# Kernel optimization log

Measured on AMD Instinct MI355X. Metric: run time of the kernel, lower is better.

The kernel has to match this reference:

```python
import jax, jax.numpy as jnp
import numpy as np

B, S, D = 2, 2048, 1024
QKV = 2048
H = 16
HD = QKV // H  # 128
SCALE = HD ** -0.5


def setup_inputs() -> dict:
    key = jax.random.key(0)
    k1, k2, k3, k4, k5 = jax.random.split(key, 5)
    std = D ** -0.5
    return {
        "x": jax.random.normal(k1, (B, S, D), dtype=jnp.float32),
        "wq": jax.random.normal(k2, (QKV, D), dtype=jnp.float32) * std,
        "wk": jax.random.normal(k3, (QKV, D), dtype=jnp.float32) * std,
        "wv": jax.random.normal(k4, (QKV, D), dtype=jnp.float32) * std,
        "wo": jax.random.normal(k5, (D, QKV), dtype=jnp.float32) * (QKV ** -0.5),
    }


def reference(x, wq, wk, wv, wo):
    b, s, _ = x.shape
    # QKV projections (torch Linear: y = x @ W.T), reshape to [b, h, s, hd]
    q = (x @ wq.T).reshape(b, s, H, HD).transpose(0, 2, 1, 3)
    k = (x @ wk.T).reshape(b, s, H, HD).transpose(0, 2, 1, 3)
    v = (x @ wv.T).reshape(b, s, H, HD).transpose(0, 2, 1, 3)
    scores = jnp.einsum("bhqd,bhkd->bhqk", q, k) * SCALE
    causal = jnp.tril(jnp.ones((s, s), dtype=bool))
    scores = jnp.where(causal[None, None], scores, -jnp.inf)
    attn = jax.nn.softmax(scores, axis=-1)  # dropout p=0 (eval)
    out = jnp.einsum("bhqk,bhkd->bhqd", attn, v)
    out = out.transpose(0, 2, 1, 3).reshape(b, s, QKV)
    return out @ wo.T
```

## Files before the change

### kernel.cpp

```cpp
#include <hip/hip_runtime.h>
#include <hip/hip_bf16.h>
#include <cstdint>

#define SEQ   2048
#define DMOD  1024
#define QKVD  2048
#define NH    16
#define HDIM  128
#define NTOK  4096

typedef __bf16 bf16;
typedef bf16 bf16x4 __attribute__((ext_vector_type(4)));
typedef bf16 bf16x8 __attribute__((ext_vector_type(8)));
typedef float f32x4 __attribute__((ext_vector_type(4)));
typedef float f32x16 __attribute__((ext_vector_type(16)));
typedef uint32_t u32x4 __attribute__((ext_vector_type(4)));

typedef __attribute__((address_space(1))) void* as1_t;
typedef __attribute__((address_space(3))) void* as3_t;

__device__ __forceinline__ void gload16(const void* g, void* l) {
  __builtin_amdgcn_global_load_lds((as1_t)(uintptr_t)g, (as3_t)(uintptr_t)l, 16, 0, 0);
}

__device__ __forceinline__ uint32_t pkbf(float a, float b) {
  union { bf16 h; unsigned short u; } x, y;
  x.h = (bf16)a; y.h = (bf16)b;
  return (uint32_t)x.u | ((uint32_t)y.u << 16);
}

__device__ __forceinline__ void plswap(uint32_t& a, uint32_t& b) {
  asm("v_permlane32_swap_b32 %0, %1" : "+v"(a), "+v"(b));
}

__global__ void cast_f32_bf16(const float* __restrict__ in, bf16* __restrict__ out, int n4) {
  int i = blockIdx.x * blockDim.x + threadIdx.x;
  if (i < n4) {
    float4 v = reinterpret_cast<const float4*>(in)[i];
    bf16x4 o;
    o[0] = (bf16)v.x; o[1] = (bf16)v.y; o[2] = (bf16)v.z; o[3] = (bf16)v.w;
    reinterpret_cast<bf16x4*>(out)[i] = o;
  }
}

__global__ void cast_w4(const float* __restrict__ p0, const float* __restrict__ p1,
                        const float* __restrict__ p2, const float* __restrict__ p3,
                        bf16* __restrict__ out) {
  int i = blockIdx.x * blockDim.x + threadIdx.x;
  const float* src = (i < 524288) ? p0 : (i < 1048576) ? p1 : (i < 1572864) ? p2 : p3;
  int off = i & 524287;
  float4 v = reinterpret_cast<const float4*>(src)[off];
  bf16x4 o;
  o[0] = (bf16)v.x; o[1] = (bf16)v.y; o[2] = (bf16)v.z; o[3] = (bf16)v.w;
  reinterpret_cast<bf16x4*>(out)[i] = o;
}

__global__ __launch_bounds__(512, 1) void qkv_gemm_kernel(
    const bf16* __restrict__ A, const bf16* __restrict__ Bw,
    bf16* __restrict__ Qo, bf16* __restrict__ Ko, bf16* __restrict__ Vto, float qs)
{
  __shared__ bf16 RING[3][24576];

  const int tid  = threadIdx.x;
  const int lane = tid & 63;
  const int wid  = tid >> 6;
  const int wm   = wid >> 2;
  const int wn   = wid & 3;
  const int lm   = lane & 15;
  const int lg   = lane >> 4;

  const int g   = blockIdx.x & 7;
  const int idx = blockIdx.x >> 3;
  const int m0  = ((g & 1) * 16 + (idx & 15)) * 128;
  const int n0  = ((g >> 1) * 6 + (idx >> 4)) * 256;

  f32x4 acc[4][4];
#pragma unroll
  for (int i = 0; i < 4; ++i)
#pragma unroll
    for (int j = 0; j < 4; ++j) acc[i][j] = (f32x4)0.0f;

  const int rl = lane >> 3;
  const int cbb = (lane & 7) * 16;

  auto stageA = [&](int kt, int slot) {
    const int k0 = kt * 64;
    char* Ab = (char*)&RING[slot][0];
#pragma unroll
    for (int r2 = 0; r2 < 2; ++r2) {
      int chunk = r2 * 8 + wid;
      int row   = chunk * 8 + rl;
      int cx    = cbb ^ ((row & 7) << 4);
      gload16(A + (size_t)(m0 + row) * DMOD + k0 + (cx >> 1), Ab + chunk * 1024);
    }
  };
  auto stageB1 = [&](int kt, int slot, int r2) {
    const int k0 = kt * 64;
    char* Bb = (char*)&RING[slot][0] + 16384;
    int chunk = r2 * 8 + wid;
    int row   = chunk * 8 + rl;
    int cx    = cbb ^ ((row & 7) << 4);
    gload16(Bw + (size_t)(n0 + row) * DMOD + k0 + (cx >> 1), Bb + chunk * 1024);
  };
  auto stageFull = [&](int kt, int slot) {
    stageA(kt, slot);
#pragma unroll
    for (int r2 = 0; r2 < 4; ++r2) stageB1(kt, slot, r2);
  };

  auto rdA = [&](const char* Ab, int mf, int kk) -> bf16x8 {
    int row = wm * 64 + mf * 16 + lm;
    int cx  = (kk * 64 + lg * 16) ^ ((row & 7) << 4);
    return *(const bf16x8*)(Ab + row * 128 + cx);
  };
  auto rdB = [&](const char* Bb, int nf, int kk) -> bf16x8 {
    int row = wn * 64 + nf * 16 + lm;
    int cx  = (kk * 64 + lg * 16) ^ ((row & 7) << 4);
    return *(const bf16x8*)(Bb + row * 128 + cx);
  };

  stageFull(0, 0);
  stageFull(1, 1);

  int cur = 0;
  for (int t = 0; t < 16; ++t) {
    if (t < 15) asm volatile("s_waitcnt vmcnt(6)" ::: "memory");
    else        asm volatile("s_waitcnt vmcnt(0)" ::: "memory");
    __builtin_amdgcn_s_barrier();

    const char* Ab = (const char*)&RING[cur][0];
    const char* Bb = Ab + 16384;
    const bool pf = (t + 2 < 16);
    const int  ps = (cur + 2 >= 3) ? (cur - 1) : (cur + 2);

    bf16x8 a[4], b[2];

#pragma unroll
    for (int mf = 0; mf < 4; ++mf) a[mf] = rdA(Ab, mf, 0);
    b[0] = rdB(Bb, 0, 0); b[1] = rdB(Bb, 1, 0);
    if (pf) stageA(t + 2, ps);
    __builtin_amdgcn_s_barrier();
    asm volatile("s_waitcnt lgkmcnt(0)" ::: "memory");
    __builtin_amdgcn_s_setprio(1);
#pragma unroll
    for (int mf = 0; mf < 4; ++mf) {
      acc[mf][0] = __builtin_amdgcn_mfma_f32_16x16x32_bf16(a[mf], b[0], acc[mf][0], 0, 0, 0);
      acc[mf][1] = __builtin_amdgcn_mfma_f32_16x16x32_bf16(a[mf], b[1], acc[mf][1], 0, 0, 0);
    }
    __builtin_amdgcn_s_setprio(0);
    __builtin_amdgcn_s_barrier();

    b[0] = rdB(Bb, 2, 0); b[1] = rdB(Bb, 3, 0);
    if (pf) { stageB1(t + 2, ps, 0); stageB1(t + 2, ps, 1); }
    __builtin_amdgcn_s_barrier();
    asm volatile("s_waitcnt lgkmcnt(0)" ::: "memory");
    __builtin_amdgcn_s_setprio(1);
#pragma unroll
    for (int mf = 0; mf < 4; ++mf) {
      acc[mf][2] = __builtin_amdgcn_mfma_f32_16x16x32_bf16(a[mf], b[0], acc[mf][2], 0, 0, 0);
      acc[mf][3] = __builtin_amdgcn_mfma_f32_16x16x32_bf16(a[mf], b[1], acc[mf][3], 0, 0, 0);
    }
    __builtin_amdgcn_s_setprio(0);
    __builtin_amdgcn_s_barrier();

#pragma unroll
    for (int mf = 0; mf < 4; ++mf) a[mf] = rdA(Ab, mf, 1);
    b[0] = rdB(Bb, 0, 1); b[1] = rdB(Bb, 1, 1);
    if (pf) stageB1(t + 2, ps, 2);
    __builtin_amdgcn_s_barrier();
    asm volatile("s_waitcnt lgkmcnt(0)" ::: "memory");
    __builtin_amdgcn_s_setprio(1);
#pragma unroll
    for (int mf = 0; mf < 4; ++mf) {
      acc[mf][0] = __builtin_amdgcn_mfma_f32_16x16x32_bf16(a[mf], b[0], acc[mf][0], 0, 0, 0);
      acc[mf][1] = __builtin_amdgcn_mfma_f32_16x16x32_bf16(a[mf], b[1], acc[mf][1], 0, 0, 0);
    }
    __builtin_amdgcn_s_setprio(0);
    __builtin_amdgcn_s_barrier();

    b[0] = rdB(Bb, 2, 1); b[1] = rdB(Bb, 3, 1);
    if (pf) stageB1(t + 2, ps, 3);
    __builtin_amdgcn_s_barrier();
    asm volatile("s_waitcnt lgkmcnt(0)" ::: "memory");
    __builtin_amdgcn_s_setprio(1);
#pragma unroll
    for (int mf = 0; mf < 4; ++mf) {
      acc[mf][2] = __builtin_amdgcn_mfma_f32_16x16x32_bf16(a[mf], b[0], acc[mf][2], 0, 0, 0);
      acc[mf][3] = __builtin_amdgcn_mfma_f32_16x16x32_bf16(a[mf], b[1], acc[mf][3], 0, 0, 0);
    }
    __builtin_amdgcn_s_setprio(0);
    __builtin_amdgcn_s_barrier();

    cur = (cur == 2) ? 0 : cur + 1;
  }

#pragma unroll
  for (int mf = 0; mf < 4; ++mf) {
#pragma unroll
    for (int nf = 0; nf < 4; ++nf) {
      int row0 = m0 + wm * 64 + mf * 16 + lg * 4;
      int col  = n0 + wn * 64 + nf * 16 + lm;
      f32x4 cv = acc[mf][nf];
      if (n0 < 2048) {
#pragma unroll
        for (int r = 0; r < 4; ++r)
          Qo[(size_t)(row0 + r) * QKVD + col] = (bf16)(cv[r] * qs);
      } else if (n0 < 4096) {
        int kc = col - 2048;
#pragma unroll
        for (int r = 0; r < 4; ++r)
          Ko[(size_t)(row0 + r) * QKVD + kc] = (bf16)cv[r];
      } else {
        int vc = col - 4096;
#pragma unroll
        for (int r = 0; r < 4; ++r) {
          int tok = row0 + r; int bb = tok >> 11; int s = tok & 2047;
          Vto[((size_t)bb * QKVD + vc) * SEQ + s] = (bf16)cv[r];
        }
      }
    }
  }
}

__global__ __launch_bounds__(256, 2) void proj_kernel(
    const bf16* __restrict__ A, const bf16* __restrict__ Bw, float* __restrict__ out)
{
  __shared__ bf16 RING[2][16384];

  const int tid  = threadIdx.x;
  const int lane = tid & 63;
  const int wid  = tid >> 6;
  const int wm   = wid >> 1;
  const int wn   = wid & 1;
  const int lm   = lane & 15;
  const int lg   = lane >> 4;

  const int g   = blockIdx.x & 7;
  const int idx = blockIdx.x >> 3;
  const int m0  = (g * 4 + (idx >> 3)) * 128;
  const int n0  = (idx & 7) * 128;

  f32x4 acc[4][4];
#pragma unroll
  for (int i = 0; i < 4; ++i)
#pragma unroll
    for (int j = 0; j < 4; ++j) acc[i][j] = (f32x4)0.0f;

  const int rl = lane >> 3;
  const int cbb = (lane & 7) * 16;

  auto stage = [&](int kt, int slot) {
    const int k0 = kt * 64;
    char* Ab = (char*)&RING[slot][0];
    char* Bb = Ab + 16384;
#pragma unroll
    for (int r2 = 0; r2 < 4; ++r2) {
      int chunk = r2 * 4 + wid;
      int row   = chunk * 8 + rl;
      int cx    = cbb ^ ((row & 7) << 4);
      gload16(A + (size_t)(m0 + row) * QKVD + k0 + (cx >> 1), Ab + chunk * 1024);
    }
#pragma unroll
    for (int r2 = 0; r2 < 4; ++r2) {
      int chunk = r2 * 4 + wid;
      int row   = chunk * 8 + rl;
      int cx    = cbb ^ ((row & 7) << 4);
      gload16(Bw + (size_t)(n0 + row) * QKVD + k0 + (cx >> 1), Bb + chunk * 1024);
    }
  };

  auto rdA = [&](const char* Ab, int mf, int kk) -> bf16x8 {
    int row = wm * 64 + mf * 16 + lm;
    int cx  = (kk * 64 + lg * 16) ^ ((row & 7) << 4);
    return *(const bf16x8*)(Ab + row * 128 + cx);
  };
  auto rdB = [&](const char* Bb, int nf, int kk) -> bf16x8 {
    int row = wn * 64 + nf * 16 + lm;
    int cx  = (kk * 64 + lg * 16) ^ ((row & 7) << 4);
    return *(const bf16x8*)(Bb + row * 128 + cx);
  };

  stage(0, 0);

  int cur = 0;
  for (int t = 0; t < 32; ++t) {
    if (t < 31) {
      stage(t + 1, cur ^ 1);
      asm volatile("s_waitcnt vmcnt(8)" ::: "memory");
    } else {
      asm volatile("s_waitcnt vmcnt(0)" ::: "memory");
    }
    __builtin_amdgcn_s_barrier();

    const char* Ab = (const char*)&RING[cur][0];
    const char* Bb = Ab + 16384;

    bf16x8 a[4], b[2];

#pragma unroll
    for (int mf = 0; mf < 4; ++mf) a[mf] = rdA(Ab, mf, 0);
    b[0] = rdB(Bb, 0, 0); b[1] = rdB(Bb, 1, 0);
    __builtin_amdgcn_s_barrier();
    asm volatile("s_waitcnt lgkmcnt(0)" ::: "memory");
    __builtin_amdgcn_s_setprio(1);
#pragma unroll
    for (int mf = 0; mf < 4; ++mf) {
      acc[mf][0] = __builtin_amdgcn_mfma_f32_16x16x32_bf16(a[mf], b[0], acc[mf][0], 0, 0, 0);
      acc[mf][1] = __builtin_amdgcn_mfma_f32_16x16x32_bf16(a[mf], b[1], acc[mf][1], 0, 0, 0);
    }
    __builtin_amdgcn_s_setprio(0);
    __builtin_amdgcn_s_barrier();

    b[0] = rdB(Bb, 2, 0); b[1] = rdB(Bb, 3, 0);
    __builtin_amdgcn_s_barrier();
    asm volatile("s_waitcnt lgkmcnt(0)" ::: "memory");
    __builtin_amdgcn_s_setprio(1);
#pragma unroll
    for (int mf = 0; mf < 4; ++mf) {
      acc[mf][2] = __builtin_amdgcn_mfma_f32_16x16x32_bf16(a[mf], b[0], acc[mf][2], 0, 0, 0);
      acc[mf][3] = __builtin_amdgcn_mfma_f32_16x16x32_bf16(a[mf], b[1], acc[mf][3], 0, 0, 0);
    }
    __builtin_amdgcn_s_setprio(0);
    __builtin_amdgcn_s_barrier();

#pragma unroll
    for (int mf = 0; mf < 4; ++mf) a[mf] = rdA(Ab, mf, 1);
    b[0] = rdB(Bb, 0, 1); b[1] = rdB(Bb, 1, 1);
    __builtin_amdgcn_s_barrier();
    asm volatile("s_waitcnt lgkmcnt(0)" ::: "memory");
    __builtin_amdgcn_s_setprio(1);
#pragma unroll
    for (int mf = 0; mf < 4; ++mf) {
      acc[mf][0] = __builtin_amdgcn_mfma_f32_16x16x32_bf16(a[mf], b[0], acc[mf][0], 0, 0, 0);
      acc[mf][1] = __builtin_amdgcn_mfma_f32_16x16x32_bf16(a[mf], b[1], acc[mf][1], 0, 0, 0);
    }
    __builtin_amdgcn_s_setprio(0);
    __builtin_amdgcn_s_barrier();

    b[0] = rdB(Bb, 2, 1); b[1] = rdB(Bb, 3, 1);
    __builtin_amdgcn_s_barrier();
    asm volatile("s_waitcnt lgkmcnt(0)" ::: "memory");
    __builtin_amdgcn_s_setprio(1);
#pragma unroll
    for (int mf = 0; mf < 4; ++mf) {
      acc[mf][2] = __builtin_amdgcn_mfma_f32_16x16x32_bf16(a[mf], b[0], acc[mf][2], 0, 0, 0);
      acc[mf][3] = __builtin_amdgcn_mfma_f32_16x16x32_bf16(a[mf], b[1], acc[mf][3], 0, 0, 0);
    }
    __builtin_amdgcn_s_setprio(0);
    __builtin_amdgcn_s_barrier();

    cur ^= 1;
  }

#pragma unroll
  for (int mf = 0; mf < 4; ++mf)
#pragma unroll
    for (int nf = 0; nf < 4; ++nf) {
      int row0 = m0 + wm * 64 + mf * 16 + lg * 4;
      int col  = n0 + wn * 64 + nf * 16 + lm;
      f32x4 cv = acc[mf][nf];
#pragma unroll
      for (int r = 0; r < 4; ++r)
        out[(size_t)(row0 + r) * DMOD + col] = cv[r];
    }
}

__global__ __launch_bounds__(256, 2) void flash_kernel(
    const bf16* __restrict__ Q, const bf16* __restrict__ Kg,
    const bf16* __restrict__ Vt, bf16* __restrict__ O)
{
  __shared__ bf16 KV[2][16384];

  const int tid  = threadIdx.x;
  const int lane = tid & 63;
  const int wid  = tid >> 6;
  const int l31  = lane & 31;
  const int lh   = lane >> 5;

  const int id  = blockIdx.x;
  const int c   = id & 255;
  const int s   = id >> 8;
  const int bh  = (c & 7) * 4 + ((c >> 3) & 3);
  const int k   = (c >> 5) & 7;
  const int T   = s ? (15 - k) : k;
  const int nu  = 2 * (T + 1);
  const int b   = bh >> 4;
  const int h   = bh & 15;
  const int rA  = T * 128 + wid * 32;

  auto stage = [&](int j, int buf) {
    bf16* kb = &KV[buf][0];
    bf16* vb = &KV[buf][8192];
    const int rb0 = wid * 16;
#pragma unroll
    for (int i = 0; i < 4; ++i) {
      int r0 = rb0 + i * 4;
      int r  = r0 + (lane >> 4);
      int cc = ((lane & 15) * 16) ^ ((r & 15) << 4);
      gload16(Kg + ((size_t)(b * SEQ + j * 64 + r)) * QKVD + h * HDIM + (cc >> 1),
              kb + r0 * 128);
    }
    const int db0 = wid * 32;
#pragma unroll
    for (int i = 0; i < 4; ++i) {
      int d0 = db0 + i * 8;
      int d  = d0 + (lane >> 3);
      int cc = ((lane & 7) * 16) ^ ((d & 7) << 4);
      gload16(Vt + ((size_t)(bh * HDIM + d)) * SEQ + j * 64 + (cc >> 1),
              vb + d0 * 64);
    }
  };

  bf16x8 qfr[8];
  {
    const bf16* qb = Q + ((size_t)(b * SEQ + rA + l31)) * QKVD + h * HDIM + lh * 8;
#pragma unroll
    for (int st = 0; st < 8; ++st) qfr[st] = *reinterpret_cast<const bf16x8*>(qb + st * 16);
  }

  f32x16 o[4];
#pragma unroll
  for (int cc = 0; cc < 4; ++cc) o[cc] = (f32x16)0.0f;
  float mreg = -__builtin_inff();
  float lreg = 0.0f;

  stage(0, 0);
  __syncthreads();

  int cur = 0;
  for (int j = 0; j < nu; ++j) {
    if (j + 1 < nu) stage(j + 1, cur ^ 1);

    const bool act = (j * 64 <= rA + 31);
    if (act) {
      const char* kbb = (const char*)&KV[cur][0];
      const char* vbb = kbb + 16384;

      f32x16 s0 = (f32x16)0.0f, s1 = (f32x16)0.0f;
#pragma unroll
      for (int st = 0; st < 8; ++st) {
        const int r0 = l31, r1 = 32 + l31;
        bf16x8 kf0 = *(const bf16x8*)(kbb + r0 * 256 + ((lh * 16 + st * 32) ^ ((r0 & 15) << 4)));
        bf16x8 kf1 = *(const bf16x8*)(kbb + r1 * 256 + ((lh * 16 + st * 32) ^ ((r1 & 15) << 4)));
        s0 = __builtin_amdgcn_mfma_f32_32x32x16_bf16(kf0, qfr[st], s0, 0, 0, 0);
        s1 = __builtin_amdgcn_mfma_f32_32x32x16_bf16(kf1, qfr[st], s1, 0, 0, 0);
      }

      const bool full = (j * 64 + 63) <= rA;
      if (!full) {
        const int qr  = rA + l31;
        const int kb0 = j * 64 + 4 * lh;
#pragma unroll
        for (int r = 0; r < 16; ++r) {
          int key = kb0 + (r & 3) + 8 * (r >> 2);
          if (key > qr)      s0[r] = -1e30f;
          if (key + 32 > qr) s1[r] = -1e30f;
        }
      }

      float mx = s0[0];
#pragma unroll
      for (int r = 1; r < 16; ++r) mx = fmaxf(mx, s0[r]);
#pragma unroll
      for (int r = 0; r < 16; ++r) mx = fmaxf(mx, s1[r]);
      mx = fmaxf(mx, __shfl_xor(mx, 32));

      float mn;
      if (__all(mx <= mreg + 8.0f)) {
        mn = mreg;
      } else {
        mn = fmaxf(mreg, mx);
        float scl = exp2f(mreg - mn);
        mreg = mn;
        lreg *= scl;
#pragma unroll
        for (int r = 0; r < 16; ++r) {
          int row = (r & 3) + 8 * (r >> 2) + 4 * lh;
          float sr = __shfl(scl, row);
#pragma unroll
          for (int cc = 0; cc < 4; ++cc) o[cc][r] *= sr;
        }
      }

      float p[32];
#pragma unroll
      for (int r = 0; r < 16; ++r) p[r]      = exp2f(s0[r] - mn);
#pragma unroll
      for (int r = 0; r < 16; ++r) p[16 + r] = exp2f(s1[r] - mn);
      float rs = 0.0f;
#pragma unroll
      for (int r = 0; r < 32; ++r) rs += p[r];
      rs += __shfl_xor(rs, 32);
      lreg += rs;

      bf16x8 pa[4];
#pragma unroll
      for (int f = 0; f < 4; ++f) {
        const float* pp = p + f * 8;
        uint32_t w0 = pkbf(pp[0], pp[1]);
        uint32_t w1 = pkbf(pp[2], pp[3]);
        uint32_t w2 = pkbf(pp[4], pp[5]);
        uint32_t w3 = pkbf(pp[6], pp[7]);
        plswap(w0, w2);
        plswap(w1, w3);
        u32x4 w = {w0, w1, w2, w3};
        pa[f] = __builtin_bit_cast(bf16x8, w);
      }

#pragma unroll
      for (int cc = 0; cc < 4; ++cc) {
        const int d = cc * 32 + l31;
        const char* vrow = vbb + d * 128;
        const int dx = (d & 7) << 4;
#pragma unroll
        for (int f = 0; f < 4; ++f) {
          bf16x8 vf = *(const bf16x8*)(vrow + ((f * 32 + lh * 16) ^ dx));
          o[cc] = __builtin_amdgcn_mfma_f32_32x32x16_bf16(pa[f], vf, o[cc], 0, 0, 0);
        }
      }
    }

    __syncthreads();
    cur ^= 1;
  }

  float linv = 1.0f / lreg;
#pragma unroll
  for (int cc = 0; cc < 4; ++cc)
#pragma unroll
    for (int r = 0; r < 16; ++r) {
      int row = (r & 3) + 8 * (r >> 2) + 4 * lh;
      float li = __shfl(linv, row);
      O[((size_t)(b * SEQ + rA + row)) * QKVD + h * HDIM + cc * 32 + l31] =
          (bf16)(o[cc][r] * li);
    }
}

extern "C" void kernel_launch(void* const* d_in, const int* in_sizes, int n_in,
                              void* d_out, int out_size, void* d_ws, size_t ws_size,
                              hipStream_t stream) {
  const float* x  = (const float*)d_in[0];
  const float* wq = (const float*)d_in[1];
  const float* wk = (const float*)d_in[2];
  const float* wv = (const float*)d_in[3];
  const float* wo = (const float*)d_in[4];
  float* out = (float*)d_out;

  bf16* xb  = (bf16*)d_ws;
  bf16* wqb = xb  + (size_t)NTOK * DMOD;
  bf16* wob = wqb + (size_t)3 * QKVD * DMOD;
  bf16* Qb  = wob + (size_t)DMOD * QKVD;
  bf16* Kb  = Qb  + (size_t)NTOK * QKVD;
  bf16* Vtb = Kb  + (size_t)NTOK * QKVD;
  bf16* Ob  = Vtb + (size_t)NTOK * QKVD;

  cast_f32_bf16<<<(NTOK * DMOD / 4) / 256, 256, 0, stream>>>(x, xb, NTOK * DMOD / 4);
  cast_w4<<<8192, 256, 0, stream>>>(wq, wk, wv, wo, wqb);

  const float qs = 0.08838834764831845f * 1.4426950408889634f;
  qkv_gemm_kernel<<<768, 512, 0, stream>>>(xb, wqb, Qb, Kb, Vtb, qs);

  flash_kernel<<<512, 256, 0, stream>>>(Qb, Kb, Vtb, Ob);

  proj_kernel<<<256, 256, 0, stream>>>(Ob, wob, out);
}
```

Before: 179.1 us.

## Enlarge QKV GEMM tile to 256x256 with double-buffered LDS

The QKV projection GEMM tile grows from 128x256 to 256x256, so each wave now computes a 128x64 sub-tile with 32 accumulators, and the grid halves to 384 blocks. The 3-slot LDS ring with a prefetch depth of 2 becomes a 2-buffer scheme that prefetches one step ahead and waits for all loads (vmcnt(0)) every iteration. Each wave holds both k-halves of its A and B fragments in registers, which raises arithmetic intensity and cuts global and LDS traffic per FLOP. The costs are more register pressure (launch bounds now ask for 2 blocks), less latency hiding from the shallower pipeline, and possible tail imbalance with 384 blocks across the CUs.

```diff
diff --git a/kernel.cpp b/kernel.cpp
--- a/kernel.cpp
+++ b/kernel.cpp
@@ -55,11 +55,11 @@
   reinterpret_cast<bf16x4*>(out)[i] = o;
 }
 
-__global__ __launch_bounds__(512, 1) void qkv_gemm_kernel(
+__global__ __launch_bounds__(512, 2) void qkv_gemm_kernel(
     const bf16* __restrict__ A, const bf16* __restrict__ Bw,
     bf16* __restrict__ Qo, bf16* __restrict__ Ko, bf16* __restrict__ Vto, float qs)
 {
-  __shared__ bf16 RING[3][24576];
+  __shared__ bf16 BUF[2][32768];
 
   const int tid  = threadIdx.x;
   const int lane = tid & 63;
@@ -71,45 +71,43 @@
 
   const int g   = blockIdx.x & 7;
   const int idx = blockIdx.x >> 3;
-  const int m0  = ((g & 1) * 16 + (idx & 15)) * 128;
-  const int n0  = ((g >> 1) * 6 + (idx >> 4)) * 256;
-
-  f32x4 acc[4][4];
-#pragma unroll
-  for (int i = 0; i < 4; ++i)
+  const int m0  = ((g & 1) * 8 + (idx & 7)) * 256;
+  const int n0  = ((g >> 1) * 6 + (idx >> 3)) * 256;
+
+  f32x4 acc[8][4];
+#pragma unroll
+  for (int i = 0; i < 8; ++i)
 #pragma unroll
     for (int j = 0; j < 4; ++j) acc[i][j] = (f32x4)0.0f;
 
-  const int rl = lane >> 3;
+  const int rl  = lane >> 3;
   const int cbb = (lane & 7) * 16;
 
-  auto stageA = [&](int kt, int slot) {
+  auto stageA2 = [&](int kt, int buf, int h) {
     const int k0 = kt * 64;
-    char* Ab = (char*)&RING[slot][0];
+    char* Ab = (char*)&BUF[buf][0];
 #pragma unroll
     for (int r2 = 0; r2 < 2; ++r2) {
-      int chunk = r2 * 8 + wid;
+      int chunk = (h * 2 + r2) * 8 + wid;
       int row   = chunk * 8 + rl;
       int cx    = cbb ^ ((row & 7) << 4);
       gload16(A + (size_t)(m0 + row) * DMOD + k0 + (cx >> 1), Ab + chunk * 1024);
     }
   };
-  auto stageB1 = [&](int kt, int slot, int r2) {
+  auto stageB2 = [&](int kt, int buf, int h) {
     const int k0 = kt * 64;
-    char* Bb = (char*)&RING[slot][0] + 16384;
-    int chunk = r2 * 8 + wid;
-    int row   = chunk * 8 + rl;
-    int cx    = cbb ^ ((row & 7) << 4);
-    gload16(Bw + (size_t)(n0 + row) * DMOD + k0 + (cx >> 1), Bb + chunk * 1024);
-  };
-  auto stageFull = [&](int kt, int slot) {
-    stageA(kt, slot);
-#pragma unroll
-    for (int r2 = 0; r2 < 4; ++r2) stageB1(kt, slot, r2);
+    char* Bb = (char*)&BUF[buf][0] + 32768;
+#pragma unroll
+    for (int r2 = 0; r2 < 2; ++r2) {
+      int chunk = (h * 2 + r2) * 8 + wid;
+      int row   = chunk * 8 + rl;
+      int cx    = cbb ^ ((row & 7) << 4);
+      gload16(Bw + (size_t)(n0 + row) * DMOD + k0 + (cx >> 1), Bb + chunk * 1024);
+    }
   };
 
   auto rdA = [&](const char* Ab, int mf, int kk) -> bf16x8 {
-    int row = wm * 64 + mf * 16 + lm;
+    int row = wm * 128 + mf * 16 + lm;
     int cx  = (kk * 64 + lg * 16) ^ ((row & 7) << 4);
     return *(const bf16x8*)(Ab + row * 128 + cx);
   };
@@ -119,86 +117,99 @@
     return *(const bf16x8*)(Bb + row * 128 + cx);
   };
 
-  stageFull(0, 0);
-  stageFull(1, 1);
-
-  int cur = 0;
+  stageA2(0, 0, 0); stageA2(0, 0, 1); stageB2(0, 0, 0); stageB2(0, 0, 1);
+
   for (int t = 0; t < 16; ++t) {
-    if (t < 15) asm volatile("s_waitcnt vmcnt(6)" ::: "memory");
-    else        asm volatile("s_waitcnt vmcnt(0)" ::: "memory");
-    __builtin_amdgcn_s_barrier();
-
-    const char* Ab = (const char*)&RING[cur][0];
-    const char* Bb = Ab + 16384;
-    const bool pf = (t + 2 < 16);
-    const int  ps = (cur + 2 >= 3) ? (cur - 1) : (cur + 2);
-
-    bf16x8 a[4], b[2];
-
-#pragma unroll
-    for (int mf = 0; mf < 4; ++mf) a[mf] = rdA(Ab, mf, 0);
-    b[0] = rdB(Bb, 0, 0); b[1] = rdB(Bb, 1, 0);
-    if (pf) stageA(t + 2, ps);
-    __builtin_amdgcn_s_barrier();
-    asm volatile("s_waitcnt lgkmcnt(0)" ::: "memory");
-    __builtin_amdgcn_s_setprio(1);
-#pragma unroll
-    for (int mf = 0; mf < 4; ++mf) {
-      acc[mf][0] = __builtin_amdgcn_mfma_f32_16x16x32_bf16(a[mf], b[0], acc[mf][0], 0, 0, 0);
-      acc[mf][1] = __builtin_amdgcn_mfma_f32_16x16x32_bf16(a[mf], b[1], acc[mf][1], 0, 0, 0);
-    }
-    __builtin_amdgcn_s_setprio(0);
-    __builtin_amdgcn_s_barrier();
-
-    b[0] = rdB(Bb, 2, 0); b[1] = rdB(Bb, 3, 0);
-    if (pf) { stageB1(t + 2, ps, 0); stageB1(t + 2, ps, 1); }
-    __builtin_amdgcn_s_barrier();
-    asm volatile("s_waitcnt lgkmcnt(0)" ::: "memory");
-    __builtin_amdgcn_s_setprio(1);
-#pragma unroll
-    for (int mf = 0; mf < 4; ++mf) {
-      acc[mf][2] = __builtin_amdgcn_mfma_f32_16x16x32_bf16(a[mf], b[0], acc[mf][2], 0, 0, 0);
-      acc[mf][3] = __builtin_amdgcn_mfma_f32_16x16x32_bf16(a[mf], b[1], acc[mf][3], 0, 0, 0);
-    }
-    __builtin_amdgcn_s_setprio(0);
-    __builtin_amdgcn_s_barrier();
-
-#pragma unroll
-    for (int mf = 0; mf < 4; ++mf) a[mf] = rdA(Ab, mf, 1);
-    b[0] = rdB(Bb, 0, 1); b[1] = rdB(Bb, 1, 1);
-    if (pf) stageB1(t + 2, ps, 2);
-    __builtin_amdgcn_s_barrier();
-    asm volatile("s_waitcnt lgkmcnt(0)" ::: "memory");
-    __builtin_amdgcn_s_setprio(1);
-#pragma unroll
-    for (int mf = 0; mf < 4; ++mf) {
-      acc[mf][0] = __builtin_amdgcn_mfma_f32_16x16x32_bf16(a[mf], b[0], acc[mf][0], 0, 0, 0);
-      acc[mf][1] = __builtin_amdgcn_mfma_f32_16x16x32_bf16(a[mf], b[1], acc[mf][1], 0, 0, 0);
-    }
-    __builtin_amdgcn_s_setprio(0);
-    __builtin_amdgcn_s_barrier();
-
-    b[0] = rdB(Bb, 2, 1); b[1] = rdB(Bb, 3, 1);
-    if (pf) stageB1(t + 2, ps, 3);
-    __builtin_amdgcn_s_barrier();
-    asm volatile("s_waitcnt lgkmcnt(0)" ::: "memory");
-    __builtin_amdgcn_s_setprio(1);
-#pragma unroll
-    for (int mf = 0; mf < 4; ++mf) {
-      acc[mf][2] = __builtin_amdgcn_mfma_f32_16x16x32_bf16(a[mf], b[0], acc[mf][2], 0, 0, 0);
-      acc[mf][3] = __builtin_amdgcn_mfma_f32_16x16x32_bf16(a[mf], b[1], acc[mf][3], 0, 0, 0);
-    }
-    __builtin_amdgcn_s_setprio(0);
-    __builtin_amdgcn_s_barrier();
-
-    cur = (cur == 2) ? 0 : cur + 1;
+    const int c = t & 1;
+    asm volatile("s_waitcnt vmcnt(0)" ::: "memory");
+    __builtin_amdgcn_s_barrier();
+
+    const char* Ab = (const char*)&BUF[c][0];
+    const char* Bb = Ab + 32768;
+    const bool pf = (t + 1 < 16);
+
+    bf16x8 a[4][2], b[2][2];
+
+#pragma unroll
+    for (int mf = 0; mf < 4; ++mf)
+#pragma unroll
+      for (int kk = 0; kk < 2; ++kk) a[mf][kk] = rdA(Ab, mf, kk);
+#pragma unroll
+    for (int nf = 0; nf < 2; ++nf)
+#pragma unroll
+      for (int kk = 0; kk < 2; ++kk) b[nf][kk] = rdB(Bb, nf, kk);
+    if (pf) { stageA2(t + 1, c ^ 1, 0); stageA2(t + 1, c ^ 1, 1); }
+    __builtin_amdgcn_s_barrier();
+    asm volatile("s_waitcnt lgkmcnt(0)" ::: "memory");
+    __builtin_amdgcn_s_setprio(1);
+#pragma unroll
+    for (int mf = 0; mf < 4; ++mf)
+#pragma unroll
+      for (int nf = 0; nf < 2; ++nf)
+#pragma unroll
+        for (int kk = 0; kk < 2; ++kk)
+          acc[mf][nf] = __builtin_amdgcn_mfma_f32_16x16x32_bf16(a[mf][kk], b[nf][kk], acc[mf][nf], 0, 0, 0);
+    __builtin_amdgcn_s_setprio(0);
+    __builtin_amdgcn_s_barrier();
+
+#pragma unroll
+    for (int nf = 0; nf < 2; ++nf)
+#pragma unroll
+      for (int kk = 0; kk < 2; ++kk) b[nf][kk] = rdB(Bb, 2 + nf, kk);
+    if (pf) { stageB2(t + 1, c ^ 1, 0); stageB2(t + 1, c ^ 1, 1); }
+    __builtin_amdgcn_s_barrier();
+    asm volatile("s_waitcnt lgkmcnt(0)" ::: "memory");
+    __builtin_amdgcn_s_setprio(1);
+#pragma unroll
+    for (int mf = 0; mf < 4; ++mf)
+#pragma unroll
+      for (int nf = 0; nf < 2; ++nf)
+#pragma unroll
+        for (int kk = 0; kk < 2; ++kk)
+          acc[mf][2 + nf] = __builtin_amdgcn_mfma_f32_16x16x32_bf16(a[mf][kk], b[nf][kk], acc[mf][2 + nf], 0, 0, 0);
+    __builtin_amdgcn_s_setprio(0);
+    __builtin_amdgcn_s_barrier();
+
+#pragma unroll
+    for (int mf = 0; mf < 4; ++mf)
+#pragma unroll
+      for (int kk = 0; kk < 2; ++kk) a[mf][kk] = rdA(Ab, 4 + mf, kk);
+    __builtin_amdgcn_s_barrier();
+    asm volatile("s_waitcnt lgkmcnt(0)" ::: "memory");
+    __builtin_amdgcn_s_setprio(1);
+#pragma unroll
+    for (int mf = 0; mf < 4; ++mf)
+#pragma unroll
+      for (int nf = 0; nf < 2; ++nf)
+#pragma unroll
+        for (int kk = 0; kk < 2; ++kk)
+          acc[4 + mf][2 + nf] = __builtin_amdgcn_mfma_f32_16x16x32_bf16(a[mf][kk], b[nf][kk], acc[4 + mf][2 + nf], 0, 0, 0);
+    __builtin_amdgcn_s_setprio(0);
+    __builtin_amdgcn_s_barrier();
+
+#pragma unroll
+    for (int nf = 0; nf < 2; ++nf)
+#pragma unroll
+      for (int kk = 0; kk < 2; ++kk) b[nf][kk] = rdB(Bb, nf, kk);
+    __builtin_amdgcn_s_barrier();
+    asm volatile("s_waitcnt lgkmcnt(0)" ::: "memory");
+    __builtin_amdgcn_s_setprio(1);
+#pragma unroll
+    for (int mf = 0; mf < 4; ++mf)
+#pragma unroll
+      for (int nf = 0; nf < 2; ++nf)
+#pragma unroll
+        for (int kk = 0; kk < 2; ++kk)
+          acc[4 + mf][nf] = __builtin_amdgcn_mfma_f32_16x16x32_bf16(a[mf][kk], b[nf][kk], acc[4 + mf][nf], 0, 0, 0);
+    __builtin_amdgcn_s_setprio(0);
+    __builtin_amdgcn_s_barrier();
   }
 
 #pragma unroll
-  for (int mf = 0; mf < 4; ++mf) {
+  for (int mf = 0; mf < 8; ++mf) {
 #pragma unroll
     for (int nf = 0; nf < 4; ++nf) {
-      int row0 = m0 + wm * 64 + mf * 16 + lg * 4;
+      int row0 = m0 + wm * 128 + mf * 16 + lg * 4;
       int col  = n0 + wn * 64 + nf * 16 + lm;
       f32x4 cv = acc[mf][nf];
       if (n0 < 2048) {
@@ -558,7 +569,7 @@
   cast_w4<<<8192, 256, 0, stream>>>(wq, wk, wv, wo, wqb);
 
   const float qs = 0.08838834764831845f * 1.4426950408889634f;
-  qkv_gemm_kernel<<<768, 512, 0, stream>>>(xb, wqb, Qb, Kb, Vtb, qs);
+  qkv_gemm_kernel<<<384, 512, 0, stream>>>(xb, wqb, Qb, Kb, Vtb, qs);
 
   flash_kernel<<<512, 256, 0, stream>>>(Qb, Kb, Vtb, Ob);
 
```

Result: no change. 179.7 us (+0.3%).

## Single-buffer V in flash attention to cut LDS and raise occupancy

Applied to the files above, without the earlier changes.

The flash kernel now double-buffers only K tiles and keeps a single V tile in LDS. V for the next step is loaded after the PV matmul and waited on with a partial vmcnt before the PV phase. This lowers LDS use from 64KB to 48KB per block so the launch bound can request three blocks per CU. It also rewrites the row max and row sum reductions as tree reductions to shorten dependency chains. The trade-off is an extra barrier per iteration and less time for the V load to hide behind compute.

```diff
diff --git a/kernel.cpp b/kernel.cpp
--- a/kernel.cpp
+++ b/kernel.cpp
@@ -365,11 +365,12 @@
     }
 }
 
-__global__ __launch_bounds__(256, 2) void flash_kernel(
+__global__ __launch_bounds__(256, 3) void flash_kernel(
     const bf16* __restrict__ Q, const bf16* __restrict__ Kg,
     const bf16* __restrict__ Vt, bf16* __restrict__ O)
 {
-  __shared__ bf16 KV[2][16384];
+  __shared__ bf16 Kl[2][8192];
+  __shared__ bf16 Vl[8192];
 
   const int tid  = threadIdx.x;
   const int lane = tid & 63;
@@ -388,9 +389,8 @@
   const int h   = bh & 15;
   const int rA  = T * 128 + wid * 32;
 
-  auto stage = [&](int j, int buf) {
-    bf16* kb = &KV[buf][0];
-    bf16* vb = &KV[buf][8192];
+  auto stageK = [&](int j, int buf) {
+    bf16* kb = &Kl[buf][0];
     const int rb0 = wid * 16;
 #pragma unroll
     for (int i = 0; i < 4; ++i) {
@@ -400,6 +400,9 @@
       gload16(Kg + ((size_t)(b * SEQ + j * 64 + r)) * QKVD + h * HDIM + (cc >> 1),
               kb + r0 * 128);
     }
+  };
+  auto stageV = [&](int j) {
+    bf16* vb = &Vl[0];
     const int db0 = wid * 32;
 #pragma unroll
     for (int i = 0; i < 4; ++i) {
@@ -424,17 +427,19 @@
   float mreg = -__builtin_inff();
   float lreg = 0.0f;
 
-  stage(0, 0);
+  stageK(0, 0);
+  stageV(0);
   __syncthreads();
 
-  int cur = 0;
   for (int j = 0; j < nu; ++j) {
-    if (j + 1 < nu) stage(j + 1, cur ^ 1);
+    const int cur = j & 1;
+    if (j + 1 < nu) stageK(j + 1, cur ^ 1);
 
     const bool act = (j * 64 <= rA + 31);
+    bf16x8 pa[4];
+
     if (act) {
-      const char* kbb = (const char*)&KV[cur][0];
-      const char* vbb = kbb + 16384;
+      const char* kbb = (const char*)&Kl[cur][0];
 
       f32x16 s0 = (f32x16)0.0f, s1 = (f32x16)0.0f;
 #pragma unroll
@@ -458,12 +463,15 @@
         }
       }
 
-      float mx = s0[0];
-#pragma unroll
-      for (int r = 1; r < 16; ++r) mx = fmaxf(mx, s0[r]);
-#pragma unroll
-      for (int r = 0; r < 16; ++r) mx = fmaxf(mx, s1[r]);
-      mx = fmaxf(mx, __shfl_xor(mx, 32));
+      float m16[16];
+#pragma unroll
+      for (int r = 0; r < 16; ++r) m16[r] = fmaxf(s0[r], s1[r]);
+#pragma unroll
+      for (int d = 8; d >= 1; d >>= 1)
+#pragma unroll
+        for (int r = 0; r < 8; ++r)
+          if (r < d) m16[r] = fmaxf(m16[r], m16[r + d]);
+      float mx = fmaxf(m16[0], __shfl_xor(m16[0], 32));
 
       float mn;
       if (__all(mx <= mreg + 8.0f)) {
@@ -487,13 +495,17 @@
       for (int r = 0; r < 16; ++r) p[r]      = exp2f(s0[r] - mn);
 #pragma unroll
       for (int r = 0; r < 16; ++r) p[16 + r] = exp2f(s1[r] - mn);
-      float rs = 0.0f;
-#pragma unroll
-      for (int r = 0; r < 32; ++r) rs += p[r];
-      rs += __shfl_xor(rs, 32);
+      float a16[16];
+#pragma unroll
+      for (int r = 0; r < 16; ++r) a16[r] = p[r] + p[16 + r];
+#pragma unroll
+      for (int d = 8; d >= 1; d >>= 1)
+#pragma unroll
+        for (int r = 0; r < 8; ++r)
+          if (r < d) a16[r] += a16[r + d];
+      float rs = a16[0] + __shfl_xor(a16[0], 32);
       lreg += rs;
 
-      bf16x8 pa[4];
 #pragma unroll
       for (int f = 0; f < 4; ++f) {
         const float* pp = p + f * 8;
@@ -506,7 +518,14 @@
         u32x4 w = {w0, w1, w2, w3};
         pa[f] = __builtin_bit_cast(bf16x8, w);
       }
-
+    }
+
+    if (j + 1 < nu) asm volatile("s_waitcnt vmcnt(4)" ::: "memory");
+    else            asm volatile("s_waitcnt vmcnt(0)" ::: "memory");
+    __builtin_amdgcn_s_barrier();
+
+    if (act) {
+      const char* vbb = (const char*)&Vl[0];
 #pragma unroll
       for (int cc = 0; cc < 4; ++cc) {
         const int d = cc * 32 + l31;
@@ -521,7 +540,7 @@
     }
 
     __syncthreads();
-    cur ^= 1;
+    if (j + 1 < nu) stageV(j + 1);
   }
 
   float linv = 1.0f / lreg;
```

New measurement: 253.8 us. 1.42x slower.

## Split flash attention KV tile across two wave groups with final softmax merge

Applied to the files above, without the earlier changes.

Doubles the flash kernel block to 512 threads, with each group of four waves processing one 32-key half of every 64-key KV tile for the same query rows. Each half keeps its own running max, sum and output accumulators. At the end, half 1 writes its partial state to shared memory and half 0 merges the two with a log-sum-exp rescale before writing the output. This doubles the waves available to hide MFMA and LDS latency and halves the per-wave serial work per tile, at the cost of an extra shared-memory reduction, a barrier, and tighter register limits from launch_bounds(512,4).

```diff
diff --git a/kernel.cpp b/kernel.cpp
--- a/kernel.cpp
+++ b/kernel.cpp
@@ -365,15 +365,18 @@
     }
 }
 
-__global__ __launch_bounds__(256, 2) void flash_kernel(
+__global__ __launch_bounds__(512, 4) void flash_kernel(
     const bf16* __restrict__ Q, const bf16* __restrict__ Kg,
     const bf16* __restrict__ Vt, bf16* __restrict__ O)
 {
   __shared__ bf16 KV[2][16384];
+  __shared__ float ML[4][64][2];
 
   const int tid  = threadIdx.x;
   const int lane = tid & 63;
   const int wid  = tid >> 6;
+  const int wg   = wid & 3;
+  const int half = wid >> 2;
   const int l31  = lane & 31;
   const int lh   = lane >> 5;
 
@@ -386,23 +389,23 @@
   const int nu  = 2 * (T + 1);
   const int b   = bh >> 4;
   const int h   = bh & 15;
-  const int rA  = T * 128 + wid * 32;
+  const int rA  = T * 128 + wg * 32;
 
   auto stage = [&](int j, int buf) {
     bf16* kb = &KV[buf][0];
     bf16* vb = &KV[buf][8192];
-    const int rb0 = wid * 16;
-#pragma unroll
-    for (int i = 0; i < 4; ++i) {
+    const int rb0 = wid * 8;
+#pragma unroll
+    for (int i = 0; i < 2; ++i) {
       int r0 = rb0 + i * 4;
       int r  = r0 + (lane >> 4);
       int cc = ((lane & 15) * 16) ^ ((r & 15) << 4);
       gload16(Kg + ((size_t)(b * SEQ + j * 64 + r)) * QKVD + h * HDIM + (cc >> 1),
               kb + r0 * 128);
     }
-    const int db0 = wid * 32;
-#pragma unroll
-    for (int i = 0; i < 4; ++i) {
+    const int db0 = wid * 16;
+#pragma unroll
+    for (int i = 0; i < 2; ++i) {
       int d0 = db0 + i * 8;
       int d  = d0 + (lane >> 3);
       int cc = ((lane & 7) * 16) ^ ((d & 7) << 4);
@@ -431,38 +434,33 @@
   for (int j = 0; j < nu; ++j) {
     if (j + 1 < nu) stage(j + 1, cur ^ 1);
 
-    const bool act = (j * 64 <= rA + 31);
+    const int k0 = j * 64 + half * 32;
+    const bool act = (k0 <= rA + 31);
     if (act) {
       const char* kbb = (const char*)&KV[cur][0];
       const char* vbb = kbb + 16384;
 
-      f32x16 s0 = (f32x16)0.0f, s1 = (f32x16)0.0f;
+      f32x16 s0 = (f32x16)0.0f;
+      const int kr = half * 32 + l31;
 #pragma unroll
       for (int st = 0; st < 8; ++st) {
-        const int r0 = l31, r1 = 32 + l31;
-        bf16x8 kf0 = *(const bf16x8*)(kbb + r0 * 256 + ((lh * 16 + st * 32) ^ ((r0 & 15) << 4)));
-        bf16x8 kf1 = *(const bf16x8*)(kbb + r1 * 256 + ((lh * 16 + st * 32) ^ ((r1 & 15) << 4)));
-        s0 = __builtin_amdgcn_mfma_f32_32x32x16_bf16(kf0, qfr[st], s0, 0, 0, 0);
-        s1 = __builtin_amdgcn_mfma_f32_32x32x16_bf16(kf1, qfr[st], s1, 0, 0, 0);
-      }
-
-      const bool full = (j * 64 + 63) <= rA;
+        bf16x8 kf = *(const bf16x8*)(kbb + kr * 256 + ((lh * 16 + st * 32) ^ ((kr & 15) << 4)));
+        s0 = __builtin_amdgcn_mfma_f32_32x32x16_bf16(kf, qfr[st], s0, 0, 0, 0);
+      }
+
+      const bool full = (k0 + 31) <= rA;
       if (!full) {
-        const int qr  = rA + l31;
-        const int kb0 = j * 64 + 4 * lh;
+        const int qr = rA + l31;
 #pragma unroll
         for (int r = 0; r < 16; ++r) {
-          int key = kb0 + (r & 3) + 8 * (r >> 2);
-          if (key > qr)      s0[r] = -1e30f;
-          if (key + 32 > qr) s1[r] = -1e30f;
+          int key = k0 + (r & 3) + 8 * (r >> 2) + 4 * lh;
+          if (key > qr) s0[r] = -1e30f;
         }
       }
 
       float mx = s0[0];
 #pragma unroll
       for (int r = 1; r < 16; ++r) mx = fmaxf(mx, s0[r]);
-#pragma unroll
-      for (int r = 0; r < 16; ++r) mx = fmaxf(mx, s1[r]);
       mx = fmaxf(mx, __shfl_xor(mx, 32));
 
       float mn;
@@ -482,20 +480,18 @@
         }
       }
 
-      float p[32];
-#pragma unroll
-      for (int r = 0; r < 16; ++r) p[r]      = exp2f(s0[r] - mn);
-#pragma unroll
-      for (int r = 0; r < 16; ++r) p[16 + r] = exp2f(s1[r] - mn);
+      float p[16];
+#pragma unroll
+      for (int r = 0; r < 16; ++r) p[r] = exp2f(s0[r] - mn);
       float rs = 0.0f;
 #pragma unroll
-      for (int r = 0; r < 32; ++r) rs += p[r];
+      for (int r = 0; r < 16; ++r) rs += p[r];
       rs += __shfl_xor(rs, 32);
       lreg += rs;
 
-      bf16x8 pa[4];
-#pragma unroll
-      for (int f = 0; f < 4; ++f) {
+      bf16x8 pa[2];
+#pragma unroll
+      for (int f = 0; f < 2; ++f) {
         const float* pp = p + f * 8;
         uint32_t w0 = pkbf(pp[0], pp[1]);
         uint32_t w1 = pkbf(pp[2], pp[3]);
@@ -513,8 +509,8 @@
         const char* vrow = vbb + d * 128;
         const int dx = (d & 7) << 4;
 #pragma unroll
-        for (int f = 0; f < 4; ++f) {
-          bf16x8 vf = *(const bf16x8*)(vrow + ((f * 32 + lh * 16) ^ dx));
+        for (int f = 0; f < 2; ++f) {
+          bf16x8 vf = *(const bf16x8*)(vrow + ((half * 64 + f * 32 + lh * 16) ^ dx));
           o[cc] = __builtin_amdgcn_mfma_f32_32x32x16_bf16(pa[f], vf, o[cc], 0, 0, 0);
         }
       }
@@ -524,16 +520,39 @@
     cur ^= 1;
   }
 
-  float linv = 1.0f / lreg;
-#pragma unroll
-  for (int cc = 0; cc < 4; ++cc)
-#pragma unroll
-    for (int r = 0; r < 16; ++r) {
-      int row = (r & 3) + 8 * (r >> 2) + 4 * lh;
-      float li = __shfl(linv, row);
-      O[((size_t)(b * SEQ + rA + row)) * QKVD + h * HDIM + cc * 32 + l31] =
-          (bf16)(o[cc][r] * li);
-    }
+  float* oex = (float*)&KV[0][0];
+  if (half == 1) {
+    float* dst = oex + (wg * 64 + lane) * 64;
+#pragma unroll
+    for (int cc = 0; cc < 4; ++cc)
+#pragma unroll
+      for (int r = 0; r < 16; ++r) dst[cc * 16 + r] = o[cc][r];
+    ML[wg][lane][0] = mreg;
+    ML[wg][lane][1] = lreg;
+  }
+  __syncthreads();
+
+  if (half == 0) {
+    float mB = ML[wg][lane][0];
+    float lB = ML[wg][lane][1];
+    float M  = fmaxf(mreg, mB);
+    float wA = exp2f(mreg - M);
+    float wB = exp2f(mB - M);
+    float linv = 1.0f / (lreg * wA + lB * wB);
+
+    const float* src = oex + (wg * 64 + lane) * 64;
+#pragma unroll
+    for (int cc = 0; cc < 4; ++cc)
+#pragma unroll
+      for (int r = 0; r < 16; ++r) {
+        int row = (r & 3) + 8 * (r >> 2) + 4 * lh;
+        float wAr = __shfl(wA, row);
+        float wBr = __shfl(wB, row);
+        float lir = __shfl(linv, row);
+        float om = (o[cc][r] * wAr + src[cc * 16 + r] * wBr) * lir;
+        O[((size_t)(b * SEQ + rA + row)) * QKVD + h * HDIM + cc * 32 + l31] = (bf16)om;
+      }
+  }
 }
 
 extern "C" void kernel_launch(void* const* d_in, const int* in_sizes, int n_in,
@@ -560,7 +579,7 @@
   const float qs = 0.08838834764831845f * 1.4426950408889634f;
   qkv_gemm_kernel<<<768, 512, 0, stream>>>(xb, wqb, Qb, Kb, Vtb, qs);
 
-  flash_kernel<<<512, 256, 0, stream>>>(Qb, Kb, Vtb, Ob);
+  flash_kernel<<<512, 512, 0, stream>>>(Qb, Kb, Vtb, Ob);
 
   proj_kernel<<<256, 256, 0, stream>>>(Ob, wob, out);
 }
```

After: 232.1 us. 29.6% more time.
